# Kernel tuning notes

Hardware: AMD Instinct MI355X
Metric: run time of the kernel (lower is better)

The kernel has to match this reference:

```python
import jax, jax.numpy as jnp
import numpy as np

# Config (matches init_kwargs): GRU decoder, score_model='default',
# local_att='False', context_vector_concat='True'. Dropout layers are
# identity (Keras eager call defaults to training=False).
B, L, FEAT = 256, 64, 2048   # batch, attention locations, feature channels
UNITS, EMB, VOCAB = 512, 256, 32000


def setup_inputs() -> dict:
    key = jax.random.key(0)
    ks = jax.random.split(key, 16)
    s = 0.02
    inp = {
        "x_tokens": jax.random.randint(ks[0], (B, 1), 0, VOCAB),
        "features": jax.random.normal(ks[1], (B, L, FEAT), jnp.float32),
        "hidden": jax.random.normal(ks[2], (B, UNITS), jnp.float32),
        # attention params
        "W1": jax.random.normal(ks[3], (FEAT, UNITS), jnp.float32) * s,
        "b1": jnp.zeros((UNITS,), jnp.float32),
        "W2": jax.random.normal(ks[4], (UNITS, UNITS), jnp.float32) * s,
        "b2": jnp.zeros((UNITS,), jnp.float32),
        "V": jax.random.normal(ks[5], (UNITS, 1), jnp.float32) * s,
        "bV": jnp.zeros((1,), jnp.float32),
        "W3": jax.random.normal(ks[6], (FEAT + UNITS, UNITS), jnp.float32) * s,
        "b3": jnp.zeros((UNITS,), jnp.float32),
        # embedding
        "emb_table": jax.random.normal(ks[7], (VOCAB, EMB), jnp.float32) * s,
        # GRU params (gate order z, r, h), input dim = UNITS + EMB
        "gru_kernel": jax.random.normal(ks[8], (UNITS + EMB, 3 * UNITS), jnp.float32) * s,
        "gru_rec": jax.random.normal(ks[9], (UNITS, 3 * UNITS), jnp.float32) * s,
        "gru_bias": jnp.zeros((3 * UNITS,), jnp.float32),
        # output heads
        "fc1_W": jax.random.normal(ks[10], (UNITS, UNITS), jnp.float32) * s,
        "fc1_b": jnp.zeros((UNITS,), jnp.float32),
        "fc2_W": jax.random.normal(ks[11], (UNITS, VOCAB), jnp.float32) * s,
        "fc2_b": jnp.zeros((VOCAB,), jnp.float32),
    }
    return inp


def _gru_step(x_t, h_prev, kernel, rec, bias):
    # Keras GRU single step (reset_after=False), gate order z, r, h.
    u = UNITS
    gx = x_t @ kernel + bias                       # [B, 3u]
    gh = h_prev @ rec                              # [B, 3u]
    z = jax.nn.sigmoid(gx[:, :u] + gh[:, :u])
    r = jax.nn.sigmoid(gx[:, u:2 * u] + gh[:, u:2 * u])
    hh = jnp.tanh(gx[:, 2 * u:] + r * gh[:, 2 * u:])
    return z * h_prev + (1.0 - z) * hh


def reference(x_tokens, features, hidden, W1, b1, W2, b2, V, bV, W3, b3,
              emb_table, gru_kernel, gru_rec, gru_bias,
              fc1_W, fc1_b, fc2_W, fc2_b):
    # Bahdanau attention, score_model='default'
    score = jnp.tanh(features @ W1 + b1 + (hidden @ W2 + b2)[:, None, :])  # [B,L,U]
    logits = score @ V + bV                                               # [B,L,1]
    attn = jax.nn.softmax(logits, axis=1)                                 # [B,L,1]
    context = jnp.sum(attn * features, axis=1)                            # [B,FEAT]
    # context_vector_concat == 'True'
    cvh = jnp.tanh(jnp.concatenate([context, hidden], axis=-1)) @ W3 + b3  # [B,U]
    # embedding + concat with context (seq len 1)
    emb = emb_table[x_tokens]                                             # [B,1,E]
    x_in = jnp.concatenate([cvh[:, None, :], emb], axis=-1)               # [B,1,U+E]
    # GRU over length-1 sequence; Keras Sequential uses zero initial state
    h0 = jnp.zeros((x_in.shape[0], UNITS), x_in.dtype)
    h_new = _gru_step(x_in[:, 0, :], h0, gru_kernel, gru_rec, gru_bias)   # [B,U]
    out = h_new[:, None, :]                                               # [B,1,U]
    x1 = out @ fc1_W + fc1_b                                              # [B,1,U]
    x1 = x1.reshape(-1, x1.shape[2])                                      # [B,U]
    logits_out = x1 @ fc2_W + fc2_b                                       # [B,VOCAB]
    return logits_out, h_new, attn
```

## Files before the change

### kernel.cpp

```cpp
#include <hip/hip_runtime.h>
#include <hip/hip_bf16.h>

#define B_N 256
#define L_Q 64
#define FEAT_N 2048
#define UNITS_N 512
#define EMB_N 256
#define VOCAB_N 32000

typedef __attribute__((ext_vector_type(8))) short bf16x8;
typedef __attribute__((ext_vector_type(4))) float f32x4;

__device__ __forceinline__ unsigned short f2bf(float x) {
  union { float f; unsigned int u; } c; c.f = x;
  unsigned int u = c.u + 0x7FFFu + ((c.u >> 16) & 1u);
  return (unsigned short)(u >> 16);
}

__device__ __forceinline__ float sigmoidf_(float x) { return 1.0f / (1.0f + __expf(-x)); }

__device__ __forceinline__ void store_frag4(unsigned short* base, int KS, int row, int k0,
                                            float a, float b, float c, float d) {
  int rt = row >> 4, lr = row & 15;
  int ks = k0 >> 5, lq = (k0 >> 3) & 3, j0 = k0 & 7;
  union { unsigned long long u; unsigned short s[4]; } p;
  p.s[0] = f2bf(a); p.s[1] = f2bf(b); p.s[2] = f2bf(c); p.s[3] = f2bf(d);
  *reinterpret_cast<unsigned long long*>(base + (((rt * KS + ks) * 64) + (lq * 16 + lr)) * 8 + j0) = p.u;
}

__device__ __forceinline__ void wfrag_one(const float* __restrict__ W, int N, int KS,
                                          unsigned short* __restrict__ dst, int tid, int gruMap) {
  int l = tid & 63;
  int ks = (tid >> 6) % KS;
  int cts = tid / (64 * KS);
  int ct = cts & 3, nt = cts >> 2;
  int nb = gruMap ? (nt < 8 ? nt * 64 : 1024 + (nt - 8) * 64) : nt * 64;
  int ncol = nb + ct * 16 + (l & 15);
  int k0 = ks * 32 + (l >> 4) * 8;
  union { bf16x8 v; unsigned short s[8]; } fr;
#pragma unroll
  for (int j = 0; j < 8; ++j) fr.s[j] = f2bf(W[(size_t)(k0 + j) * N + ncol]);
  *reinterpret_cast<bf16x8*>(dst + (size_t)tid * 8) = fr.v;
}

__global__ void k_prep_all(const float* __restrict__ W1, unsigned short* __restrict__ W1s,
                           const float* __restrict__ hidden,
                           const float* __restrict__ emb_table,
                           const int* __restrict__ tok,
                           unsigned short* __restrict__ hfrag,
                           unsigned short* __restrict__ xinfrag,
                           const float* __restrict__ W2, unsigned short* __restrict__ W2f,
                           const float* __restrict__ W3, unsigned short* __restrict__ W3f,
                           const float* __restrict__ gruK, unsigned short* __restrict__ gruf,
                           const float* __restrict__ fc1W, unsigned short* __restrict__ fc1f) {
  int bb = blockIdx.x;
  if (bb < 512) {
    int t = bb * 256 + threadIdx.x;
    int l = t & 63;
    int c = (t >> 6) & 31;
    int kt = t >> 11;
    int n = c * 16 + (l & 15);
    int k0 = kt * 32 + (l >> 4) * 8;
    union { bf16x8 v; unsigned short s[8]; } fr;
#pragma unroll
    for (int j = 0; j < 8; ++j) fr.s[j] = f2bf(W1[(size_t)(k0 + j) * UNITS_N + n]);
    *reinterpret_cast<bf16x8*>(W1s + (size_t)t * 8) = fr.v;
  } else if (bb < 704) {
    int t = (bb - 512) * 256 + threadIdx.x;
    if (t < 32768) {
      int b = t >> 7, k0 = (t & 127) * 4;
      const float* s = hidden + (size_t)b * UNITS_N + k0;
      store_frag4(hfrag, 16, b, k0, s[0], s[1], s[2], s[3]);
    } else if (t < 49152) {
      int t2 = t - 32768;
      int b = t2 >> 6, e0 = (t2 & 63) * 4;
      const float* s = emb_table + (size_t)tok[b] * EMB_N + e0;
      store_frag4(xinfrag, 24, b, 512 + e0, s[0], s[1], s[2], s[3]);
    }
  } else if (bb < 832) {
    wfrag_one(W2, 512, 16, W2f, (bb - 704) * 256 + threadIdx.x, 0);
  } else if (bb < 1472) {
    wfrag_one(W3, 512, 80, W3f, (bb - 832) * 256 + threadIdx.x, 0);
  } else if (bb < 1856) {
    wfrag_one(gruK, 1536, 24, gruf, (bb - 1472) * 256 + threadIdx.x, 1);
  } else {
    wfrag_one(fc1W, 512, 16, fc1f, (bb - 1856) * 256 + threadIdx.x, 0);
  }
}

template <int MODE>
__launch_bounds__(256)
__global__ void k_small2(const unsigned short* __restrict__ Afrag, int KS,
                         const unsigned short* __restrict__ Bfrag,
                         const float* __restrict__ bias,
                         float* __restrict__ outF, int N,
                         unsigned short* __restrict__ outFrag, int KSo) {
  constexpr int NCT = (MODE == 2) ? 8 : 4;
  __shared__ f32x4 red[4][2][NCT][64];
  int t = threadIdx.x, w = t >> 6, l = t & 63;
  int nt = blockIdx.x;
  int mb = blockIdx.y;
  int KSq = KS >> 2;

  f32x4 acc[2][NCT];
#pragma unroll
  for (int rt = 0; rt < 2; ++rt)
#pragma unroll
    for (int ct = 0; ct < NCT; ++ct) acc[rt][ct] = (f32x4){0.f, 0.f, 0.f, 0.f};

  for (int s = 0; s < KSq; ++s) {
    int ks = w * KSq + s;
    bf16x8 af[2];
#pragma unroll
    for (int rt = 0; rt < 2; ++rt)
      af[rt] = *reinterpret_cast<const bf16x8*>(Afrag + (((size_t)(mb * 2 + rt) * KS + ks) * 64 + l) * 8);
#pragma unroll
    for (int ct = 0; ct < NCT; ++ct) {
      int tile = (MODE == 2) ? (ct < 4 ? nt : 8 + nt) : nt;
      int cts = ct & 3;
      bf16x8 bf = *reinterpret_cast<const bf16x8*>(Bfrag + (((size_t)(tile * 4 + cts) * KS + ks) * 64 + l) * 8);
#pragma unroll
      for (int rt = 0; rt < 2; ++rt)
        acc[rt][ct] = __builtin_amdgcn_mfma_f32_16x16x32_bf16(af[rt], bf, acc[rt][ct], 0, 0, 0);
    }
  }

#pragma unroll
  for (int rt = 0; rt < 2; ++rt)
#pragma unroll
    for (int ct = 0; ct < NCT; ++ct) red[w][rt][ct][l] = acc[rt][ct];
  __syncthreads();

#pragma unroll
  for (int si = 0; si < 2; ++si) {
    int s = t + si * 256;
    int l2 = s & 63, ct = (s >> 6) & 3, rt = s >> 8;
    f32x4 v = red[0][rt][ct][l2];
#pragma unroll
    for (int ww = 1; ww < 4; ++ww) v += red[ww][rt][ct][l2];
    int col = nt * 64 + ct * 16 + (l2 & 15);
    int row0 = mb * 32 + rt * 16 + (l2 >> 4) * 4;
    if (MODE == 2) {
      f32x4 vh = red[0][rt][ct + 4][l2];
#pragma unroll
      for (int ww = 1; ww < 4; ++ww) vh += red[ww][rt][ct + 4][l2];
      float bz = bias[col], bh = bias[1024 + col];
#pragma unroll
      for (int i = 0; i < 4; ++i) {
        float hv = (1.f - sigmoidf_(v[i] + bz)) * tanhf(vh[i] + bh);
        int row = row0 + i;
        outF[(size_t)row * UNITS_N + col] = hv;
        int k = col;
        outFrag[(((size_t)(row >> 4) * KSo + (k >> 5)) * 64 + (((k >> 3) & 3) * 16 + (row & 15))) * 8 + (k & 7)] = f2bf(hv);
      }
    } else {
      float bv = bias[col];
#pragma unroll
      for (int i = 0; i < 4; ++i) {
        float vv = v[i] + bv;
        int row = row0 + i;
        if (MODE == 0) {
          outF[(size_t)row * N + col] = vv;
        } else {
          int k = col;
          outFrag[(((size_t)(row >> 4) * KSo + (k >> 5)) * 64 + (((k >> 3) & 3) * 16 + (row & 15))) * 8 + (k & 7)] = f2bf(vv);
        }
      }
    }
  }
}

__launch_bounds__(512, 2)
__global__ void k_gemm1f(const float* __restrict__ features,
                         const unsigned short* __restrict__ W1s,
                         const float* __restrict__ hproj,
                         const float* __restrict__ b1,
                         const float* __restrict__ V,
                         const float* __restrict__ hidden,
                         float* __restrict__ attn_out,
                         unsigned short* __restrict__ tcfrag) {
  __shared__ float wlog[8][32];
  __shared__ float aL[64];

  int b = blockIdx.x;
  int t = threadIdx.x, w = t >> 6, l = t & 63;
  int wr = w >> 2, wc = w & 3;

  f32x4 acc[2][8];
#pragma unroll
  for (int rt = 0; rt < 2; ++rt)
#pragma unroll
    for (int ct = 0; ct < 8; ++ct) acc[rt][ct] = (f32x4){0.f, 0.f, 0.f, 0.f};

  const float* Arow = features + ((size_t)(b * 64 + wr * 32 + (l & 15))) * FEAT_N + ((l >> 4) * 8);
  const unsigned short* Bcol = W1s + ((size_t)(wc * 8) * 64 + l) * 8;

  for (int kt = 0; kt < 64; ++kt) {
    bf16x8 af[2];
#pragma unroll
    for (int rt = 0; rt < 2; ++rt) {
      const float* p = Arow + (size_t)rt * 16 * FEAT_N + kt * 32;
      float4 x0 = *reinterpret_cast<const float4*>(p);
      float4 x1 = *reinterpret_cast<const float4*>(p + 4);
      union { bf16x8 v; unsigned short s[8]; } u;
      u.s[0] = f2bf(x0.x); u.s[1] = f2bf(x0.y); u.s[2] = f2bf(x0.z); u.s[3] = f2bf(x0.w);
      u.s[4] = f2bf(x1.x); u.s[5] = f2bf(x1.y); u.s[6] = f2bf(x1.z); u.s[7] = f2bf(x1.w);
      af[rt] = u.v;
    }
#pragma unroll
    for (int ct = 0; ct < 8; ++ct) {
      bf16x8 bv = *reinterpret_cast<const bf16x8*>(Bcol + ((size_t)(kt * 32 + ct) * 64) * 8);
      acc[0][ct] = __builtin_amdgcn_mfma_f32_16x16x32_bf16(af[0], bv, acc[0][ct], 0, 0, 0);
      acc[1][ct] = __builtin_amdgcn_mfma_f32_16x16x32_bf16(af[1], bv, acc[1][ct], 0, 0, 0);
    }
  }

  float rowpart[8];
#pragma unroll
  for (int i = 0; i < 8; ++i) rowpart[i] = 0.f;
#pragma unroll
  for (int ct = 0; ct < 8; ++ct) {
    int col = (wc * 8 + ct) * 16 + (l & 15);
    float hb = hproj[(size_t)b * UNITS_N + col] + b1[col];
    float vv = V[col];
#pragma unroll
    for (int rt = 0; rt < 2; ++rt)
#pragma unroll
      for (int i = 0; i < 4; ++i)
        rowpart[rt * 4 + i] += tanhf(acc[rt][ct][i] + hb) * vv;
  }
#pragma unroll
  for (int m = 1; m <= 8; m <<= 1)
#pragma unroll
    for (int i = 0; i < 8; ++i) rowpart[i] += __shfl_xor(rowpart[i], m, 64);
  if ((l & 15) == 0) {
    int g = l >> 4;
#pragma unroll
    for (int rt = 0; rt < 2; ++rt)
#pragma unroll
      for (int i = 0; i < 4; ++i)
        wlog[w][rt * 16 + g * 4 + i] = rowpart[rt * 4 + i];
  }
  __syncthreads();
  if (t < 64) {
    int wr2 = t >> 5, rl = t & 31;
    float x = wlog[wr2 * 4 + 0][rl] + wlog[wr2 * 4 + 1][rl] +
              wlog[wr2 * 4 + 2][rl] + wlog[wr2 * 4 + 3][rl];
    float mx = x;
#pragma unroll
    for (int m = 1; m < 64; m <<= 1) mx = fmaxf(mx, __shfl_xor(mx, m, 64));
    float e = __expf(x - mx);
    float s = e;
#pragma unroll
    for (int m = 1; m < 64; m <<= 1) s += __shfl_xor(s, m, 64);
    float a = e / s;
    aL[t] = a;
    attn_out[(size_t)b * 64 + t] = a;
  }
  __syncthreads();

  {
    const float* F = features + (size_t)b * 64 * FEAT_N + t * 4;
    float a0 = 0.f, a1 = 0.f, a2 = 0.f, a3 = 0.f;
#pragma unroll 4
    for (int lr = 0; lr < 64; ++lr) {
      float4 f = *reinterpret_cast<const float4*>(F + (size_t)lr * FEAT_N);
      float av = aL[lr];
      a0 += av * f.x; a1 += av * f.y; a2 += av * f.z; a3 += av * f.w;
    }
    store_frag4(tcfrag, 80, b, t * 4, tanhf(a0), tanhf(a1), tanhf(a2), tanhf(a3));
  }
  if (t < 128) {
    const float* H = hidden + (size_t)b * UNITS_N + t * 4;
    store_frag4(tcfrag, 80, b, 2048 + t * 4, tanhf(H[0]), tanhf(H[1]), tanhf(H[2]), tanhf(H[3]));
  }
}

__launch_bounds__(256)
__global__ void k_fc2(const unsigned short* __restrict__ x1frag,
                      const float* __restrict__ W, const float* __restrict__ bias,
                      float* __restrict__ out) {
  __shared__ unsigned short Bb[4 * 64 * 8];
  int t = threadIdx.x, w = t >> 6, l = t & 63;
  int n0 = blockIdx.x * 64;
  int mh = blockIdx.y;
  f32x4 acc[2][4];
#pragma unroll
  for (int r = 0; r < 2; ++r)
#pragma unroll
    for (int c = 0; c < 4; ++c) acc[r][c] = (f32x4){0.f, 0.f, 0.f, 0.f};

  int sn = t & 63, kc = t >> 6;
  unsigned short* wdst = &Bb[(((sn >> 4) * 64) + ((sn & 15) | (kc << 4))) * 8];
  const float* Wp = W + n0 + sn;
  float wreg[8];
#pragma unroll
  for (int j = 0; j < 8; ++j) wreg[j] = Wp[(size_t)(kc * 8 + j) * VOCAB_N];

  for (int kt = 0; kt < 16; ++kt) {
    __syncthreads();
    {
      union { bf16x8 v; unsigned short s[8]; } p;
#pragma unroll
      for (int j = 0; j < 8; ++j) p.s[j] = f2bf(wreg[j]);
      *reinterpret_cast<bf16x8*>(wdst) = p.v;
    }
    __syncthreads();
    if (kt < 15) {
#pragma unroll
      for (int j = 0; j < 8; ++j) wreg[j] = Wp[(size_t)((kt + 1) * 32 + kc * 8 + j) * VOCAB_N];
    }
    bf16x8 bf[4];
#pragma unroll
    for (int c = 0; c < 4; ++c) bf[c] = *reinterpret_cast<const bf16x8*>(&Bb[((c * 64) + l) * 8]);
#pragma unroll
    for (int rti = 0; rti < 2; ++rti) {
      int rtg = mh * 8 + w * 2 + rti;
      bf16x8 af = *reinterpret_cast<const bf16x8*>(x1frag + ((size_t)(rtg * 16 + kt) * 64 + l) * 8);
#pragma unroll
      for (int c = 0; c < 4; ++c)
        acc[rti][c] = __builtin_amdgcn_mfma_f32_16x16x32_bf16(af, bf[c], acc[rti][c], 0, 0, 0);
    }
  }
#pragma unroll
  for (int c = 0; c < 4; ++c) {
    int col = n0 + c * 16 + (l & 15);
    float bv = bias[col];
#pragma unroll
    for (int rti = 0; rti < 2; ++rti)
#pragma unroll
      for (int i = 0; i < 4; ++i) {
        int row = mh * 128 + w * 32 + rti * 16 + (l >> 4) * 4 + i;
        out[(size_t)row * VOCAB_N + col] = acc[rti][c][i] + bv;
      }
  }
}

extern "C" void kernel_launch(void* const* d_in, const int* in_sizes, int n_in,
                              void* d_out, int out_size, void* d_ws, size_t ws_size,
                              hipStream_t stream) {
  const int*   tok        = (const int*)d_in[0];
  const float* features   = (const float*)d_in[1];
  const float* hidden     = (const float*)d_in[2];
  const float* W1         = (const float*)d_in[3];
  const float* b1         = (const float*)d_in[4];
  const float* W2         = (const float*)d_in[5];
  const float* b2         = (const float*)d_in[6];
  const float* V          = (const float*)d_in[7];
  const float* W3         = (const float*)d_in[9];
  const float* b3         = (const float*)d_in[10];
  const float* emb_table  = (const float*)d_in[11];
  const float* gru_kernel = (const float*)d_in[12];
  const float* gru_bias   = (const float*)d_in[14];
  const float* fc1_W      = (const float*)d_in[15];
  const float* fc1_b      = (const float*)d_in[16];
  const float* fc2_W      = (const float*)d_in[17];
  const float* fc2_b      = (const float*)d_in[18];

  float* out_logits = (float*)d_out;
  float* out_h      = out_logits + (size_t)B_N * VOCAB_N;
  float* out_attn   = out_h + (size_t)B_N * UNITS_N;

  char* ws = (char*)d_ws;
  unsigned short* W1s     = (unsigned short*)(ws);
  float*          hproj   = (float*)(ws + 2097152);
  unsigned short* hfrag   = (unsigned short*)(ws + 2621440);
  unsigned short* tcfrag  = (unsigned short*)(ws + 2883584);
  unsigned short* xinfrag = (unsigned short*)(ws + 4194304);
  unsigned short* hnfrag  = (unsigned short*)(ws + 4587520);
  unsigned short* x1frag  = (unsigned short*)(ws + 4849664);
  unsigned short* W2f     = (unsigned short*)(ws + 5242880);
  unsigned short* W3f     = (unsigned short*)(ws + 5767168);
  unsigned short* gruf    = (unsigned short*)(ws + 8388608);
  unsigned short* fc1f    = (unsigned short*)(ws + 9961472);

  k_prep_all<<<dim3(1984), dim3(256), 0, stream>>>(W1, W1s, hidden, emb_table, tok,
                                                   hfrag, xinfrag, W2, W2f, W3, W3f,
                                                   gru_kernel, gruf, fc1_W, fc1f);
  k_small2<0><<<dim3(8, 8), dim3(256), 0, stream>>>(hfrag, 16, W2f, b2, hproj, 512,
                                                    (unsigned short*)nullptr, 0);
  k_gemm1f<<<dim3(256), dim3(512), 0, stream>>>(features, W1s, hproj, b1, V, hidden,
                                                out_attn, tcfrag);
  k_small2<1><<<dim3(8, 8), dim3(256), 0, stream>>>(tcfrag, 80, W3f, b3, (float*)nullptr, 0,
                                                    xinfrag, 24);
  k_small2<2><<<dim3(8, 8), dim3(256), 0, stream>>>(xinfrag, 24, gruf, gru_bias, out_h, 512,
                                                    hnfrag, 16);
  k_small2<1><<<dim3(8, 8), dim3(256), 0, stream>>>(hnfrag, 16, fc1f, fc1_b, (float*)nullptr, 0,
                                                    x1frag, 16);
  k_fc2<<<dim3(500, 2), dim3(256), 0, stream>>>(x1frag, fc2_W, fc2_b, out_logits);
}
```

Measured before the change: 175.8 us.

## Stage W1 B-fragments into LDS via async global_load_lds double buffering

In the attention GEMM kernel, each wave no longer reads its W1 bf16 fragments straight from global memory. The 16-tile halves of each k-step are now staged into a shared LDS buffer with global_load_lds, split across the two buffers and shared by all waves of the block. The column-tile assignment per wave changes to match the halves, and the epilogue column mapping is updated to fit. This cuts redundant global/L2 traffic for W1 and overlaps the fetches with MFMA work, at the cost of two block barriers per k-step.

Result: slower. 206.3 us (+17.3%).

```diff
diff --git a/kernel.cpp b/kernel.cpp
--- a/kernel.cpp
+++ b/kernel.cpp
@@ -26,6 +26,13 @@
   union { unsigned long long u; unsigned short s[4]; } p;
   p.s[0] = f2bf(a); p.s[1] = f2bf(b); p.s[2] = f2bf(c); p.s[3] = f2bf(d);
   *reinterpret_cast<unsigned long long*>(base + (((rt * KS + ks) * 64) + (lq * 16 + lr)) * 8 + j0) = p.u;
+}
+
+__device__ __forceinline__ void gload_lds16(const void* g, void* lds) {
+  __builtin_amdgcn_global_load_lds(
+      (const __attribute__((address_space(1))) unsigned int*)(uintptr_t)g,
+      (__attribute__((address_space(3))) unsigned int*)(unsigned)(uintptr_t)lds,
+      16, 0, 0);
 }
 
 __device__ __forceinline__ void wfrag_one(const float* __restrict__ W, int N, int KS,
@@ -179,6 +186,7 @@
                          const float* __restrict__ hidden,
                          float* __restrict__ attn_out,
                          unsigned short* __restrict__ tcfrag) {
+  __shared__ unsigned short Bb[2][16 * 64 * 8];
   __shared__ float wlog[8][32];
   __shared__ float aL[64];
 
@@ -193,26 +201,53 @@
     for (int ct = 0; ct < 8; ++ct) acc[rt][ct] = (f32x4){0.f, 0.f, 0.f, 0.f};
 
   const float* Arow = features + ((size_t)(b * 64 + wr * 32 + (l & 15))) * FEAT_N + ((l >> 4) * 8);
-  const unsigned short* Bcol = W1s + ((size_t)(wc * 8) * 64 + l) * 8;
+  const char* W1c = (const char*)W1s;
+
+#pragma unroll
+  for (int i = 0; i < 2; ++i)
+    gload_lds16(W1c + ((size_t)(0 * 32 + 0 + w * 2 + i) << 10) + (size_t)l * 16,
+                (char*)Bb[0] + ((w * 2 + i) << 10));
+  __syncthreads();
 
   for (int kt = 0; kt < 64; ++kt) {
+    float4 x0a = *reinterpret_cast<const float4*>(Arow + kt * 32);
+    float4 x1a = *reinterpret_cast<const float4*>(Arow + kt * 32 + 4);
+    float4 x0b = *reinterpret_cast<const float4*>(Arow + (size_t)16 * FEAT_N + kt * 32);
+    float4 x1b = *reinterpret_cast<const float4*>(Arow + (size_t)16 * FEAT_N + kt * 32 + 4);
+#pragma unroll
+    for (int i = 0; i < 2; ++i)
+      gload_lds16(W1c + ((size_t)(kt * 32 + 16 + w * 2 + i) << 10) + (size_t)l * 16,
+                  (char*)Bb[1] + ((w * 2 + i) << 10));
     bf16x8 af[2];
-#pragma unroll
-    for (int rt = 0; rt < 2; ++rt) {
-      const float* p = Arow + (size_t)rt * 16 * FEAT_N + kt * 32;
-      float4 x0 = *reinterpret_cast<const float4*>(p);
-      float4 x1 = *reinterpret_cast<const float4*>(p + 4);
+    {
       union { bf16x8 v; unsigned short s[8]; } u;
-      u.s[0] = f2bf(x0.x); u.s[1] = f2bf(x0.y); u.s[2] = f2bf(x0.z); u.s[3] = f2bf(x0.w);
-      u.s[4] = f2bf(x1.x); u.s[5] = f2bf(x1.y); u.s[6] = f2bf(x1.z); u.s[7] = f2bf(x1.w);
-      af[rt] = u.v;
-    }
-#pragma unroll
-    for (int ct = 0; ct < 8; ++ct) {
-      bf16x8 bv = *reinterpret_cast<const bf16x8*>(Bcol + ((size_t)(kt * 32 + ct) * 64) * 8);
-      acc[0][ct] = __builtin_amdgcn_mfma_f32_16x16x32_bf16(af[0], bv, acc[0][ct], 0, 0, 0);
-      acc[1][ct] = __builtin_amdgcn_mfma_f32_16x16x32_bf16(af[1], bv, acc[1][ct], 0, 0, 0);
-    }
+      u.s[0] = f2bf(x0a.x); u.s[1] = f2bf(x0a.y); u.s[2] = f2bf(x0a.z); u.s[3] = f2bf(x0a.w);
+      u.s[4] = f2bf(x1a.x); u.s[5] = f2bf(x1a.y); u.s[6] = f2bf(x1a.z); u.s[7] = f2bf(x1a.w);
+      af[0] = u.v;
+      u.s[0] = f2bf(x0b.x); u.s[1] = f2bf(x0b.y); u.s[2] = f2bf(x0b.z); u.s[3] = f2bf(x0b.w);
+      u.s[4] = f2bf(x1b.x); u.s[5] = f2bf(x1b.y); u.s[6] = f2bf(x1b.z); u.s[7] = f2bf(x1b.w);
+      af[1] = u.v;
+    }
+#pragma unroll
+    for (int ct = 0; ct < 4; ++ct) {
+      bf16x8 bfr = *reinterpret_cast<const bf16x8*>(&Bb[0][((wc * 4 + ct) * 64 + l) * 8]);
+      acc[0][ct] = __builtin_amdgcn_mfma_f32_16x16x32_bf16(af[0], bfr, acc[0][ct], 0, 0, 0);
+      acc[1][ct] = __builtin_amdgcn_mfma_f32_16x16x32_bf16(af[1], bfr, acc[1][ct], 0, 0, 0);
+    }
+    __syncthreads();
+    if (kt + 1 < 64) {
+#pragma unroll
+      for (int i = 0; i < 2; ++i)
+        gload_lds16(W1c + ((size_t)((kt + 1) * 32 + w * 2 + i) << 10) + (size_t)l * 16,
+                    (char*)Bb[0] + ((w * 2 + i) << 10));
+    }
+#pragma unroll
+    for (int ct = 0; ct < 4; ++ct) {
+      bf16x8 bfr = *reinterpret_cast<const bf16x8*>(&Bb[1][((wc * 4 + ct) * 64 + l) * 8]);
+      acc[0][4 + ct] = __builtin_amdgcn_mfma_f32_16x16x32_bf16(af[0], bfr, acc[0][4 + ct], 0, 0, 0);
+      acc[1][4 + ct] = __builtin_amdgcn_mfma_f32_16x16x32_bf16(af[1], bfr, acc[1][4 + ct], 0, 0, 0);
+    }
+    __syncthreads();
   }
 
   float rowpart[8];
@@ -220,7 +255,7 @@
   for (int i = 0; i < 8; ++i) rowpart[i] = 0.f;
 #pragma unroll
   for (int ct = 0; ct < 8; ++ct) {
-    int col = (wc * 8 + ct) * 16 + (l & 15);
+    int col = (ct < 4 ? wc * 64 + ct * 16 : 256 + wc * 64 + (ct - 4) * 16) + (l & 15);
     float hb = hproj[(size_t)b * UNITS_N + col] + b1[col];
     float vv = V[col];
 #pragma unroll
```
